# Kernel optimization log

Measured on AMD Instinct MI355X. Metric: run time of the kernel, lower is better.

Reference implementation:

```python
import jax, jax.numpy as jnp
import numpy as np

DEG2RAD = np.float32(np.pi / 180.0)


def _rot(theta_deg, axis):
    # pytorch3d RotateAxisAngle uses degrees
    t = theta_deg[0] * DEG2RAD
    c, s = jnp.cos(t), jnp.sin(t)
    one, zero = jnp.ones_like(c), jnp.zeros_like(c)
    if axis == 'X':
        rows = [one, zero, zero, zero, c, -s, zero, s, c]
    elif axis == 'Y':
        rows = [c, zero, s, zero, one, zero, -s, zero, c]
    else:
        rows = [c, -s, zero, s, c, zero, zero, zero, one]
    return jnp.stack(rows).reshape(3, 3)


def _sample(verts, faces, fidx, uv):
    # gather sampled triangles: [N,3,3]
    tri = verts[faces[fidx]]
    v0, v1, v2 = tri[:, 0], tri[:, 1], tri[:, 2]
    # pytorch3d barycentric parametrization: w0=1-sqrt(u), w1=sqrt(u)(1-v), w2=sqrt(u)v
    su = jnp.sqrt(uv[:, 0:1])
    v = uv[:, 1:2]
    pts = (1.0 - su) * v0 + su * (1.0 - v) * v1 + su * v * v2
    n = jnp.cross(v1 - v0, v2 - v0)
    n = n / (jnp.linalg.norm(n, axis=-1, keepdims=True) + 1e-8)
    return pts, n


def _chamfer(x, y, nx, ny):
    # brute-force pairwise squared distances [N,M]
    d2 = (jnp.sum(x * x, -1)[:, None] + jnp.sum(y * y, -1)[None, :]
          - 2.0 * (x @ y.T))
    ixy = jnp.argmin(d2, axis=1)
    iyx = jnp.argmin(d2, axis=0)
    cham_x = jnp.take_along_axis(d2, ixy[:, None], axis=1)[:, 0]
    cham_y = jnp.take_along_axis(d2, iyx[None, :], axis=0)[0, :]
    loss_c = cham_x.mean() + cham_y.mean()
    # normals term: 1 - |cos| at nearest neighbors (pytorch3d abs_cosine=True)
    cos_x = jnp.abs(jnp.sum(nx * ny[ixy], axis=-1))
    cos_y = jnp.abs(jnp.sum(ny * nx[iyx], axis=-1))
    loss_n = (1.0 - cos_x).mean() + (1.0 - cos_y).mean()
    return loss_c + loss_n


def setup_inputs() -> dict:
    key = jax.random.key(0)
    ks = jax.random.split(key, 12)
    V, F, N = 40000, 80000, 10000
    return {
        'verts_mov': jax.random.normal(ks[0], (V, 3), jnp.float32),
        'faces_mov': jax.random.randint(ks[1], (F, 3), 0, V, jnp.int32),
        'verts_fix': jax.random.normal(ks[2], (V, 3), jnp.float32),
        'faces_fix': jax.random.randint(ks[3], (F, 3), 0, V, jnp.int32),
        'translation': jax.random.normal(ks[4], (1, 3), jnp.float32),
        'angle_x': jax.random.normal(ks[5], (1,), jnp.float32),
        'angle_y': jax.random.normal(ks[6], (1,), jnp.float32),
        'angle_z': jax.random.normal(ks[7], (1,), jnp.float32),
        'fidx_mov': jax.random.randint(ks[8], (N,), 0, F, jnp.int32),
        'uv_mov': jax.random.uniform(ks[9], (N, 2), jnp.float32),
        'fidx_fix': jax.random.randint(ks[10], (N,), 0, F, jnp.int32),
        'uv_fix': jax.random.uniform(ks[11], (N, 2), jnp.float32),
    }


def reference(verts_mov, faces_mov, verts_fix, faces_fix, translation,
              angle_x, angle_y, angle_z, fidx_mov, uv_mov, fidx_fix, uv_fix):
    # rigid transform: translate then rotate about X, Y, Z (degrees)
    p = verts_mov + translation
    p = p @ _rot(angle_x, 'X').T
    p = p @ _rot(angle_y, 'Y').T
    p = p @ _rot(angle_z, 'Z').T
    pts_m, n_m = _sample(p, faces_mov, fidx_mov, uv_mov)
    pts_f, n_f = _sample(verts_fix, faces_fix, fidx_fix, uv_fix)
    loss = _chamfer(pts_m, pts_f, n_m, n_f)
    return (loss, p)
```

## Files before the change

### kernel.cpp

```cpp
#include <hip/hip_runtime.h>
#include <math.h>

#define NJ  64
#define CB  256
#define IPT 4
#define CHUNK_MAX (((10000 + NJ - 1) / NJ) + 8)

__device__ __forceinline__ void xform(float x, float y, float z,
                                      float tx, float ty, float tz,
                                      float cx, float sx, float cy, float sy,
                                      float cz, float sz,
                                      float& ox, float& oy, float& oz)
{
    x += tx; y += ty; z += tz;
    float x1 = x;
    float y1 = cx*y - sx*z;
    float z1 = sx*y + cx*z;
    float x2 =  cy*x1 + sy*z1;
    float y2 = y1;
    float z2 = -sy*x1 + cy*z1;
    ox = cz*x2 - sz*y2;
    oy = sz*x2 + cz*y2;
    oz = z2;
}

__global__ void k_prep(const float* __restrict__ vertsM, const int* __restrict__ facesM,
                       const int* __restrict__ fidxM, const float* __restrict__ uvM,
                       float4* __restrict__ ptsM, float4* __restrict__ nrmM,
                       const float* __restrict__ vertsF, const int* __restrict__ facesF,
                       const int* __restrict__ fidxF, const float* __restrict__ uvF,
                       float4* __restrict__ ptsF, float4* __restrict__ nrmF,
                       const float* __restrict__ trans,
                       const float* __restrict__ ax,
                       const float* __restrict__ ay,
                       const float* __restrict__ az,
                       float* __restrict__ lossOut,
                       float* __restrict__ pOut,
                       int V, int N, int nbT, int nbS)
{
    const float D2R = 0.017453292519943295f;
    int b = blockIdx.x;

    if (b == 0 && threadIdx.x == 0) lossOut[0] = 0.0f;

    if (b < nbT) {
        int i = b * blockDim.x + threadIdx.x;
        if (i >= V) return;
        float txr = ax[0]*D2R, tyr = ay[0]*D2R, tzr = az[0]*D2R;
        float cx = cosf(txr), sx = sinf(txr);
        float cy = cosf(tyr), sy = sinf(tyr);
        float cz = cosf(tzr), sz = sinf(tzr);
        float ox, oy, oz;
        xform(vertsM[3*i+0], vertsM[3*i+1], vertsM[3*i+2],
              trans[0], trans[1], trans[2], cx, sx, cy, sy, cz, sz, ox, oy, oz);
        pOut[3*i+0] = ox; pOut[3*i+1] = oy; pOut[3*i+2] = oz;
        return;
    }

    int bb = b - nbT;
    int which = (bb >= nbS) ? 1 : 0;
    int bx = which ? bb - nbS : bb;
    int i = bx * blockDim.x + threadIdx.x;
    if (i >= N) return;

    const float* verts = which ? vertsF : vertsM;
    const int*   faces = which ? facesF : facesM;
    const int*   fidx  = which ? fidxF  : fidxM;
    const float* uv    = which ? uvF    : uvM;
    float4* ptsS = which ? ptsF : ptsM;
    float4* nrm  = which ? nrmF : nrmM;

    int f  = fidx[i];
    int i0 = faces[3*f+0], i1 = faces[3*f+1], i2 = faces[3*f+2];
    float v0x = verts[3*i0+0], v0y = verts[3*i0+1], v0z = verts[3*i0+2];
    float v1x = verts[3*i1+0], v1y = verts[3*i1+1], v1z = verts[3*i1+2];
    float v2x = verts[3*i2+0], v2y = verts[3*i2+1], v2z = verts[3*i2+2];

    if (!which) {
        float txr = ax[0]*D2R, tyr = ay[0]*D2R, tzr = az[0]*D2R;
        float cx = cosf(txr), sx = sinf(txr);
        float cy = cosf(tyr), sy = sinf(tyr);
        float cz = cosf(tzr), sz = sinf(tzr);
        xform(v0x,v0y,v0z, trans[0],trans[1],trans[2], cx,sx,cy,sy,cz,sz, v0x,v0y,v0z);
        xform(v1x,v1y,v1z, trans[0],trans[1],trans[2], cx,sx,cy,sy,cz,sz, v1x,v1y,v1z);
        xform(v2x,v2y,v2z, trans[0],trans[1],trans[2], cx,sx,cy,sy,cz,sz, v2x,v2y,v2z);
    }

    float su = sqrtf(uv[2*i+0]);
    float vv = uv[2*i+1];
    float a = 1.0f - su;
    float bq = su * (1.0f - vv);
    float c = su * vv;
    float px = a*v0x + bq*v1x + c*v2x;
    float py = a*v0y + bq*v1y + c*v2y;
    float pz = a*v0z + bq*v1z + c*v2z;

    float e1x = v1x - v0x, e1y = v1y - v0y, e1z = v1z - v0z;
    float e2x = v2x - v0x, e2y = v2y - v0y, e2z = v2z - v0z;
    float nx = e1y*e2z - e1z*e2y;
    float ny = e1z*e2x - e1x*e2z;
    float nz = e1x*e2y - e1y*e2x;
    float nn = sqrtf(nx*nx + ny*ny + nz*nz) + 1e-8f;
    nx /= nn; ny /= nn; nz /= nn;

    ptsS[i] = make_float4(px, py, pz, px*px + py*py + pz*pz);
    nrm[i]  = make_float4(nx, ny, nz, 0.0f);
}

__global__ void k_cham2(const float4* __restrict__ Pm, const float4* __restrict__ Pf,
                        float* __restrict__ pv, int N)
{
    int dir = blockIdx.z;
    const float4* X = dir ? Pf : Pm;
    const float4* Y = dir ? Pm : Pf;
    float* out = pv + (size_t)dir * NJ * N;

    __shared__ float4 tile[CHUNK_MAX];
    int chunk = blockIdx.y;
    int j0 = (int)(((long long)N * chunk) / NJ);
    int j1 = (int)(((long long)N * (chunk + 1)) / NJ);
    int cnt = j1 - j0;
    for (int t = threadIdx.x; t < cnt; t += CB) tile[t] = Y[j0 + t];
    if (threadIdx.x < 2) tile[cnt + threadIdx.x] = make_float4(0.f, 0.f, 0.f, 3.4e38f);
    __syncthreads();

    int ibase = blockIdx.x * CB * IPT + threadIdx.x;

    float xs0[IPT], xs1[IPT], xs2[IPT];
    #pragma unroll
    for (int p = 0; p < IPT; ++p) {
        int i = ibase + p * CB;
        float4 x = (i < N) ? X[i] : make_float4(0.f, 0.f, 0.f, 0.f);
        xs0[p] = -2.0f * x.x;
        xs1[p] = -2.0f * x.y;
        xs2[p] = -2.0f * x.z;
    }
    float best[IPT];
    #pragma unroll
    for (int p = 0; p < IPT; ++p) best[p] = 3.4e38f;

    int cnt2 = (cnt + 1) & ~1;
    #pragma unroll 2
    for (int jj = 0; jj < cnt2; jj += 2) {
        float4 y0 = tile[jj];
        float4 y1 = tile[jj + 1];
        #pragma unroll
        for (int p = 0; p < IPT; ++p) {
            float d0 = fmaf(xs0[p], y0.x, fmaf(xs1[p], y0.y, fmaf(xs2[p], y0.z, y0.w)));
            float d1 = fmaf(xs0[p], y1.x, fmaf(xs1[p], y1.y, fmaf(xs2[p], y1.z, y1.w)));
            best[p] = fminf(fminf(d0, d1), best[p]);
        }
    }
    #pragma unroll
    for (int p = 0; p < IPT; ++p) {
        int i = ibase + p * CB;
        if (i < N) out[(size_t)chunk*N + i] = best[p];
    }
}

__global__ void k_combine(const float* __restrict__ pv,
                          const float4* __restrict__ Pm, const float4* __restrict__ Pf,
                          const float4* __restrict__ n_m, const float4* __restrict__ n_f,
                          float* __restrict__ lossOut, float invN, int N)
{
    int dir = blockIdx.y;
    const float*  pvd = pv + (size_t)dir * NJ * N;
    const float4* Xp  = dir ? Pf : Pm;
    const float4* Yp  = dir ? Pm : Pf;

    int i = blockIdx.x * 256 + threadIdx.x;
    float term = 0.0f;
    if (i < N) {
        float best = 3.4e38f; int bc = 0;
        #pragma unroll
        for (int c = 0; c < NJ; ++c) {
            float v = pvd[(size_t)c*N + i];
            if (v < best) { best = v; bc = c; }
        }
        float4 x = Xp[i];
        float xs0 = -2.0f*x.x, xs1 = -2.0f*x.y, xs2 = -2.0f*x.z;
        int j0 = (int)(((long long)N * bc) / NJ);
        int j1 = (int)(((long long)N * (bc + 1)) / NJ);
        float bd = 3.4e38f; int bj = j0;
        for (int j = j0; j < j1; ++j) {
            float4 y = Yp[j];
            float d = fmaf(xs0, y.x, fmaf(xs1, y.y, fmaf(xs2, y.z, y.w)));
            if (d < bd) { bd = d; bj = j; }
        }
        float4 a = dir ? n_f[i]  : n_m[i];
        float4 b = dir ? n_m[bj] : n_f[bj];
        term = (best + x.w) + 1.0f - fabsf(a.x*b.x + a.y*b.y + a.z*b.z);
    }
    __shared__ float red[256];
    red[threadIdx.x] = term;
    __syncthreads();
    for (int s = 128; s > 0; s >>= 1) {
        if (threadIdx.x < s) red[threadIdx.x] += red[threadIdx.x + s];
        __syncthreads();
    }
    if (threadIdx.x == 0) atomicAdd(lossOut, red[0] * invN);
}

extern "C" void kernel_launch(void* const* d_in, const int* in_sizes, int n_in,
                              void* d_out, int out_size, void* d_ws, size_t ws_size,
                              hipStream_t stream)
{
    const float* verts_mov = (const float*)d_in[0];
    const int*   faces_mov = (const int*)  d_in[1];
    const float* verts_fix = (const float*)d_in[2];
    const int*   faces_fix = (const int*)  d_in[3];
    const float* trans     = (const float*)d_in[4];
    const float* ax        = (const float*)d_in[5];
    const float* ay        = (const float*)d_in[6];
    const float* az        = (const float*)d_in[7];
    const int*   fidx_mov  = (const int*)  d_in[8];
    const float* uv_mov    = (const float*)d_in[9];
    const int*   fidx_fix  = (const int*)  d_in[10];
    const float* uv_fix    = (const float*)d_in[11];

    int V = in_sizes[0] / 3;
    int N = in_sizes[8];

    float* out = (float*)d_out;
    float* p   = out + 1;

    float*  ws      = (float*)d_ws;
    float4* ptsS_m  = (float4*)(ws + 0*4*N);
    float4* n_m     = (float4*)(ws + 1*4*N);
    float4* ptsS_f  = (float4*)(ws + 2*4*N);
    float4* n_f     = (float4*)(ws + 3*4*N);
    float*  pv      = ws + 16*N;

    int nbT = (V + 255) / 256;
    int nbS = (N + 255) / 256;
    k_prep<<<nbT + 2*nbS, 256, 0, stream>>>(verts_mov, faces_mov, fidx_mov, uv_mov,
                                            ptsS_m, n_m,
                                            verts_fix, faces_fix, fidx_fix, uv_fix,
                                            ptsS_f, n_f,
                                            trans, ax, ay, az, out, p, V, N, nbT, nbS);

    dim3 gc((N + CB*IPT - 1)/(CB*IPT), NJ, 2);
    k_cham2<<<gc, CB, 0, stream>>>(ptsS_m, ptsS_f, pv, N);

    int GX = (N + 255)/256;
    dim3 gk(GX, 2);
    k_combine<<<gk, 256, 0, stream>>>(pv, ptsS_m, ptsS_f, n_m, n_f, out, 1.0f/(float)N, N);
}
```

Baseline: 128.0 us.

## Parallelize combine step with one wave per query point

k_combine now assigns a 64-lane wave to each query point. Each lane reads one chunk's partial minimum, a wave shuffle reduction picks the best chunk, and the lanes then split that chunk's rescan and reduce again with shuffles. This replaces a serial 64-iteration loop and a serial ~157-point rescan per thread, which suffered divergent, uncoalesced loads. The cost is far more threads, 1250 blocks of 1024, and a strided pv read pattern where each lane touches a different row.

```diff
diff --git a/kernel.cpp b/kernel.cpp
--- a/kernel.cpp
+++ b/kernel.cpp
@@ -5,6 +5,8 @@
 #define CB  256
 #define IPT 4
 #define CHUNK_MAX (((10000 + NJ - 1) / NJ) + 8)
+
+static_assert(NJ == 64, "k_combine maps chunks onto the 64 lanes of a wave");
 
 __device__ __forceinline__ void xform(float x, float y, float z,
                                       float tx, float ty, float tz,
@@ -158,47 +160,66 @@
     }
 }
 
-__global__ void k_combine(const float* __restrict__ pv,
-                          const float4* __restrict__ Pm, const float4* __restrict__ Pf,
-                          const float4* __restrict__ n_m, const float4* __restrict__ n_f,
-                          float* __restrict__ lossOut, float invN, int N)
+__global__ __launch_bounds__(1024)
+void k_combine(const float* __restrict__ pv,
+               const float4* __restrict__ Pm, const float4* __restrict__ Pf,
+               const float4* __restrict__ n_m, const float4* __restrict__ n_f,
+               float* __restrict__ lossOut, float invN, int N)
 {
     int dir = blockIdx.y;
     const float*  pvd = pv + (size_t)dir * NJ * N;
     const float4* Xp  = dir ? Pf : Pm;
     const float4* Yp  = dir ? Pm : Pf;
 
-    int i = blockIdx.x * 256 + threadIdx.x;
+    int wid  = threadIdx.x >> 6;
+    int lane = threadIdx.x & 63;
+    int i    = blockIdx.x * 16 + wid;
+
     float term = 0.0f;
     if (i < N) {
-        float best = 3.4e38f; int bc = 0;
-        #pragma unroll
-        for (int c = 0; c < NJ; ++c) {
-            float v = pvd[(size_t)c*N + i];
-            if (v < best) { best = v; bc = c; }
-        }
+        float v  = pvd[(size_t)lane * N + i];
+        int   bc = lane;
+        #pragma unroll
+        for (int off = 32; off > 0; off >>= 1) {
+            float ov = __shfl_down(v, off, 64);
+            int   oc = __shfl_down(bc, off, 64);
+            if (ov < v || (ov == v && oc < bc)) { v = ov; bc = oc; }
+        }
+        v  = __shfl(v, 0, 64);
+        bc = __shfl(bc, 0, 64);
+
         float4 x = Xp[i];
         float xs0 = -2.0f*x.x, xs1 = -2.0f*x.y, xs2 = -2.0f*x.z;
         int j0 = (int)(((long long)N * bc) / NJ);
         int j1 = (int)(((long long)N * (bc + 1)) / NJ);
-        float bd = 3.4e38f; int bj = j0;
-        for (int j = j0; j < j1; ++j) {
+        float bd = 3.4e38f; int bj = 0x7fffffff;
+        for (int j = j0 + lane; j < j1; j += 64) {
             float4 y = Yp[j];
             float d = fmaf(xs0, y.x, fmaf(xs1, y.y, fmaf(xs2, y.z, y.w)));
             if (d < bd) { bd = d; bj = j; }
         }
-        float4 a = dir ? n_f[i]  : n_m[i];
-        float4 b = dir ? n_m[bj] : n_f[bj];
-        term = (best + x.w) + 1.0f - fabsf(a.x*b.x + a.y*b.y + a.z*b.z);
-    }
-    __shared__ float red[256];
-    red[threadIdx.x] = term;
+        #pragma unroll
+        for (int off = 32; off > 0; off >>= 1) {
+            float od = __shfl_down(bd, off, 64);
+            int   oj = __shfl_down(bj, off, 64);
+            if (od < bd || (od == bd && oj < bj)) { bd = od; bj = oj; }
+        }
+        if (lane == 0) {
+            float4 a = dir ? n_f[i]  : n_m[i];
+            float4 b = dir ? n_m[bj] : n_f[bj];
+            term = (v + x.w) + 1.0f - fabsf(a.x*b.x + a.y*b.y + a.z*b.z);
+        }
+    }
+
+    __shared__ float red[16];
+    if (lane == 0) red[wid] = term;
     __syncthreads();
-    for (int s = 128; s > 0; s >>= 1) {
-        if (threadIdx.x < s) red[threadIdx.x] += red[threadIdx.x + s];
-        __syncthreads();
-    }
-    if (threadIdx.x == 0) atomicAdd(lossOut, red[0] * invN);
+    if (threadIdx.x == 0) {
+        float s = 0.0f;
+        #pragma unroll
+        for (int w = 0; w < 16; ++w) s += red[w];
+        atomicAdd(lossOut, s * invN);
+    }
 }
 
 extern "C" void kernel_launch(void* const* d_in, const int* in_sizes, int n_in,
@@ -242,7 +263,6 @@
     dim3 gc((N + CB*IPT - 1)/(CB*IPT), NJ, 2);
     k_cham2<<<gc, CB, 0, stream>>>(ptsS_m, ptsS_f, pv, N);
 
-    int GX = (N + 255)/256;
-    dim3 gk(GX, 2);
-    k_combine<<<gk, 256, 0, stream>>>(pv, ptsS_m, ptsS_f, n_m, n_f, out, 1.0f/(float)N, N);
-}
+    dim3 gk((N + 15)/16, 2);
+    k_combine<<<gk, 1024, 0, stream>>>(pv, ptsS_m, ptsS_f, n_m, n_f, out, 1.0f/(float)N, N);
+}
```

After: 121.9 us. 4.8% less time.
